# Optimization experiments

Hardware: AMD Instinct MI355X
Metric: run time of the kernel (lower is better)

The kernel has to match this reference:

```python
import jax, jax.numpy as jnp
import numpy as np

PAD = 1  # PAD_token; embedding rows at PAD are zero (padding_idx)


def setup_inputs() -> dict:
    V, D, HOPS = 50000, 128, 3
    B, Lc, Mc = 16, 256, 8
    Lk, Mk = 512, 8
    key = jax.random.key(0)
    kC, kK, kc, kk = jax.random.split(key, 4)
    # one table per hop (C_0..C_{HOPS-1}, K_0..K_{HOPS-1}), init N(0, 0.1)
    C = 0.1 * jax.random.normal(kC, (HOPS, V, D), dtype=jnp.float32)
    K = 0.1 * jax.random.normal(kK, (HOPS, V, D), dtype=jnp.float32)
    C = C.at[:, PAD].set(0.0)
    K = K.at[:, PAD].set(0.0)
    conv_seqs = jax.random.randint(kc, (B, Lc, Mc), 0, V)
    kb_arr = jax.random.randint(kk, (B, Lk, Mk), 0, V)  # dense, PAD-padded ragged KB
    return {"conv_seqs": conv_seqs, "kb_arr": kb_arr, "C": C, "K": K}


def reference(conv_seqs, kb_arr, C, K):
    B, Lc, _ = conv_seqs.shape
    HOPS, _, D = C.shape
    conv_feature = jnp.zeros((B, Lc, D), dtype=C.dtype)
    for hop in range(HOPS):
        # embedding-bag: gather + sum over span tokens
        cf = jnp.sum(C[hop][conv_seqs], axis=2)  # [B, Lc, D]
        kf = jnp.sum(K[hop][kb_arr], axis=2)     # [B, Lk, D]
        att = jnp.einsum('bld,bkd->blk', cf, kf)  # [B, Lc, Lk]
        p = jax.nn.softmax(att, axis=-1)
        conv_feature = jnp.einsum('blk,bkd->bld', p, kf) + conv_feature
    return conv_feature.transpose(1, 0, 2)  # [Lc, B, D]
```

## Files before the change

kernel.cpp:

```cpp
#include <hip/hip_runtime.h>

#define V_    50000
#define D_    128
#define HOPS_ 3
#define B_    16
#define LC_   256
#define MC_   8
#define LK_   512
#define MK_   8

typedef __bf16  bf16x8  __attribute__((ext_vector_type(8)));
typedef unsigned short ushort8 __attribute__((ext_vector_type(8)));
typedef unsigned short ushort4v __attribute__((ext_vector_type(4)));
typedef float   floatx4 __attribute__((ext_vector_type(4)));

__device__ inline unsigned short f2bf(float f) {
    union { float f; unsigned u; } x; x.f = f;
    unsigned r = x.u + 0x7FFFu + ((x.u >> 16) & 1u);
    return (unsigned short)(r >> 16);
}

__device__ inline floatx4 mfma_bf16(ushort8 a, ushort8 b, floatx4 c) {
    return __builtin_amdgcn_mfma_f32_16x16x32_bf16(
        __builtin_bit_cast(bf16x8, a), __builtin_bit_cast(bf16x8, b), c, 0, 0, 0);
}

__global__ __launch_bounds__(256, 6) void gather_kernel(
    const int* __restrict__ kb_arr, const float* __restrict__ Kt,
    unsigned short* __restrict__ kf, unsigned short* __restrict__ kfT,
    float4* __restrict__ out4)
{
    __shared__ unsigned short tile[16][136];

    const int tid  = threadIdx.x;
    const int bx   = blockIdx.x;

    constexpr int KBLK = HOPS_ * B_ * (LK_ / 16);

    if (bx >= KBLK) {
        out4[(size_t)(bx - KBLK) * 256 + tid] = make_float4(0.f, 0.f, 0.f, 0.f);
        return;
    }

    const int r    = tid >> 4;
    const int s    = tid & 15;
    const int lane = tid & 63;

    const int hop  = bx / (B_ * 32);
    const int rem  = bx % (B_ * 32);
    const int b    = rem >> 5;
    const int row0 = (rem & 31) * 16;
    const int g    = hop * B_ + b;

    const int* idxp = kb_arr + (size_t)(b * LK_ + row0 + r) * MK_;
    const float* table = Kt + (size_t)hop * V_ * D_;
    unsigned short* dst = kf + ((size_t)g * LK_ + row0 + r) * D_;

    const int myidx = idxp[s & 7];
    int idxs[8];
    #pragma unroll
    for (int m = 0; m < 8; ++m)
        idxs[m] = __shfl(myidx, (lane & 48) + m);

    float4 a0 = make_float4(0.f, 0.f, 0.f, 0.f);
    float4 a1 = make_float4(0.f, 0.f, 0.f, 0.f);

    #pragma unroll
    for (int m = 0; m < 8; ++m) {
        const float4* rowp = (const float4*)(table + (size_t)idxs[m] * D_);
        float4 v0 = rowp[s * 2];
        float4 v1 = rowp[s * 2 + 1];
        a0.x += v0.x; a0.y += v0.y; a0.z += v0.z; a0.w += v0.w;
        a1.x += v1.x; a1.y += v1.y; a1.z += v1.z; a1.w += v1.w;
    }

    ushort8 o;
    o[0] = f2bf(a0.x); o[1] = f2bf(a0.y); o[2] = f2bf(a0.z); o[3] = f2bf(a0.w);
    o[4] = f2bf(a1.x); o[5] = f2bf(a1.y); o[6] = f2bf(a1.z); o[7] = f2bf(a1.w);
    *(ushort8*)(dst + s * 8) = o;

    *(ushort8*)&tile[r][s * 8] = o;
    __syncthreads();
    const int d    = tid >> 1;
    const int half = tid & 1;
    unsigned short* tdst = kfT + ((size_t)g * D_ + d) * LK_ + row0 + half * 8;
    ushort8 t8;
    #pragma unroll
    for (int i = 0; i < 8; ++i) t8[i] = tile[half * 8 + i][d];
    *(ushort8*)(tdst) = t8;
}

__global__ __launch_bounds__(512) void attn_kernel(
    const int* __restrict__ conv_seqs, const float* __restrict__ Ct,
    const unsigned short* __restrict__ kf, const unsigned short* __restrict__ kfT,
    float* __restrict__ out)
{
    constexpr int AS = 516;
    constexpr int PS = 520;
    __shared__ float att_s[16][AS];
    __shared__ unsigned short p_s[16][PS];
    __shared__ float rowinv_s[16];

    unsigned short* cf_s = &p_s[0][0];

    const int tid  = threadIdx.x;
    const int wave = tid >> 6;
    const int lane = tid & 63;
    const int quad = lane >> 4;
    const int l16  = lane & 15;

    const int gl  = blockIdx.x & 7;
    const int s_  = blockIdx.x >> 3;
    const int lt  = s_ / 6;
    const int gh  = s_ % 6;
    const int g   = gh * 8 + gl;
    const int hop = g >> 4;
    const int b   = g & 15;
    const int l0  = lt * 16;

    const unsigned short* kf_h  = kf  + ((size_t)g) * 512 * 128;
    const unsigned short* kfT_h = kfT + ((size_t)g) * 128 * 512;

    {
        const int bag = tid >> 5;
        const int sl  = tid & 31;
        const int d0  = sl * 4;
        const int* idxp = conv_seqs + (size_t)(b * LC_ + l0 + bag) * MC_;
        const float* table = Ct + (size_t)hop * V_ * D_;
        float4 acc = make_float4(0.f, 0.f, 0.f, 0.f);
        #pragma unroll
        for (int m = 0; m < 8; ++m) {
            const float4 v = *(const float4*)(table + (size_t)idxp[m] * D_ + d0);
            acc.x += v.x; acc.y += v.y; acc.z += v.z; acc.w += v.w;
        }
        ushort4v oc;
        oc[0] = f2bf(acc.x); oc[1] = f2bf(acc.y);
        oc[2] = f2bf(acc.z); oc[3] = f2bf(acc.w);
        *(ushort4v*)&cf_s[bag * 132 + d0] = oc;
    }
    __syncthreads();

    ushort8 afrag[4];
    #pragma unroll
    for (int ks = 0; ks < 4; ++ks)
        afrag[ks] = *(const ushort8*)&cf_s[l16 * 132 + ks * 32 + quad * 8];

    #pragma unroll
    for (int t = 0; t < 4; ++t) {
        const int nt = wave * 4 + t;
        floatx4 acc = {0.f, 0.f, 0.f, 0.f};
        #pragma unroll
        for (int ks = 0; ks < 4; ++ks) {
            ushort8 bfrag = *(const ushort8*)(kf_h + (nt * 16 + l16) * 128 + ks * 32 + quad * 8);
            acc = mfma_bf16(afrag[ks], bfrag, acc);
        }
        #pragma unroll
        for (int rr = 0; rr < 4; ++rr)
            att_s[quad * 4 + rr][nt * 16 + l16] = acc[rr];
    }
    __syncthreads();

    #pragma unroll
    for (int rr = 0; rr < 2; ++rr) {
        const int row = wave * 2 + rr;
        float v[8];
        float mx = -1e30f;
        #pragma unroll
        for (int j = 0; j < 8; ++j) {
            v[j] = att_s[row][lane + j * 64];
            mx = fmaxf(mx, v[j]);
        }
        #pragma unroll
        for (int off = 32; off; off >>= 1) mx = fmaxf(mx, __shfl_xor(mx, off));
        float sum = 0.f;
        #pragma unroll
        for (int j = 0; j < 8; ++j) {
            float e = __expf(v[j] - mx);
            p_s[row][lane + j * 64] = f2bf(e);
            sum += e;
        }
        #pragma unroll
        for (int off = 32; off; off >>= 1) sum += __shfl_xor(sum, off);
        if (lane == 0) rowinv_s[row] = 1.0f / sum;
    }
    __syncthreads();

    floatx4 pacc = {0.f, 0.f, 0.f, 0.f};
    #pragma unroll
    for (int ks = 0; ks < 16; ++ks) {
        ushort8 pa    = *(const ushort8*)&p_s[l16][ks * 32 + quad * 8];
        ushort8 bfrag = *(const ushort8*)(kfT_h + (size_t)(wave * 16 + l16) * 512 + ks * 32 + quad * 8);
        pacc = mfma_bf16(pa, bfrag, pacc);
    }

    const int d = wave * 16 + l16;
    #pragma unroll
    for (int rr = 0; rr < 4; ++rr)
        atomicAdd(&out[(((size_t)(l0 + quad * 4 + rr)) * 16 + b) * 128 + d],
                  pacc[rr] * rowinv_s[quad * 4 + rr]);
}

extern "C" void kernel_launch(void* const* d_in, const int* in_sizes, int n_in,
                              void* d_out, int out_size, void* d_ws, size_t ws_size,
                              hipStream_t stream) {
    (void)in_sizes; (void)n_in; (void)out_size; (void)ws_size;
    const int*   conv_seqs = (const int*)d_in[0];
    const int*   kb_arr    = (const int*)d_in[1];
    const float* C         = (const float*)d_in[2];
    const float* K         = (const float*)d_in[3];

    unsigned short* kf  = (unsigned short*)d_ws;
    unsigned short* kfT = kf + (size_t)HOPS_ * B_ * LK_ * D_;
    float* out = (float*)d_out;

    hipLaunchKernelGGL(gather_kernel, dim3(2048), dim3(256), 0, stream,
                       kb_arr, K, kf, kfT, (float4*)out);
    hipLaunchKernelGGL(attn_kernel, dim3(768), dim3(512), 0, stream,
                       conv_seqs, C, kf, kfT, out);
}
```

Before: 189.6 us.

## Fuse KB gather and attention into one cooperative kernel with grid sync

Merges the KB embedding-bag gather, the output zeroing and the attention kernel into a single cooperative launch of 768 blocks. Each block gathers 32 KB rows plus its own 16 conversation bags, then a grid-wide barrier separates gather from attention. The aim is to remove the second launch and the gap between kernels, and to overlap the conv gather with the KB gather. The cost is a grid sync, a requirement that all 768 blocks of 512 threads be co-resident, and a fallback to the two-kernel path if the cooperative launch fails.

```diff
diff --git a/kernel.cpp b/kernel.cpp
--- a/kernel.cpp
+++ b/kernel.cpp
@@ -1,4 +1,7 @@
 #include <hip/hip_runtime.h>
+#include <hip/hip_cooperative_groups.h>
+
+namespace cg = cooperative_groups;
 
 #define V_    50000
 #define D_    128
@@ -23,6 +26,169 @@
 __device__ inline floatx4 mfma_bf16(ushort8 a, ushort8 b, floatx4 c) {
     return __builtin_amdgcn_mfma_f32_16x16x32_bf16(
         __builtin_bit_cast(bf16x8, a), __builtin_bit_cast(bf16x8, b), c, 0, 0, 0);
+}
+
+__global__ __launch_bounds__(512, 6) void fused_kernel(
+    const int* __restrict__ conv_seqs, const int* __restrict__ kb_arr,
+    const float* __restrict__ Ct, const float* __restrict__ Kt,
+    unsigned short* __restrict__ kf, unsigned short* __restrict__ kfT,
+    float* __restrict__ out)
+{
+    constexpr int AS = 516;
+    constexpr int PS = 520;
+    __shared__ float att_s[16][AS];
+    __shared__ unsigned short p_s[16][PS];
+    __shared__ float rowinv_s[16];
+
+    unsigned short* cf_s = (unsigned short*)&att_s[0][0];
+    unsigned short (*tile2)[136] = (unsigned short (*)[136])&p_s[0][0];
+
+    const int tid  = threadIdx.x;
+    const int wave = tid >> 6;
+    const int lane = tid & 63;
+    const int quad = lane >> 4;
+    const int l16  = lane & 15;
+
+    const int gl  = blockIdx.x & 7;
+    const int s_  = blockIdx.x >> 3;
+    const int lt  = s_ / 6;
+    const int gh  = s_ % 6;
+    const int g   = gh * 8 + gl;
+    const int hop = g >> 4;
+    const int b   = g & 15;
+    const int l0  = lt * 16;
+    const int row0 = lt * 32;
+
+    {
+        const int zi = blockIdx.x * 512 + tid;
+        if (zi < LC_ * B_ * D_ / 4)
+            reinterpret_cast<float4*>(out)[zi] = make_float4(0.f, 0.f, 0.f, 0.f);
+    }
+
+    {
+        const int r = tid >> 4;
+        const int s = tid & 15;
+        const int* idxp = kb_arr + (size_t)(b * LK_ + row0 + r) * MK_;
+        const float* table = Kt + (size_t)hop * V_ * D_;
+        unsigned short* dst = kf + ((size_t)g * LK_ + row0 + r) * D_;
+
+        const int myidx = idxp[s & 7];
+        int idxs[8];
+        #pragma unroll
+        for (int m = 0; m < 8; ++m)
+            idxs[m] = __shfl(myidx, (lane & 48) + m);
+
+        float4 a0 = make_float4(0.f, 0.f, 0.f, 0.f);
+        float4 a1 = make_float4(0.f, 0.f, 0.f, 0.f);
+        #pragma unroll
+        for (int m = 0; m < 8; ++m) {
+            const float4* rowp = (const float4*)(table + (size_t)idxs[m] * D_);
+            float4 v0 = rowp[s * 2];
+            float4 v1 = rowp[s * 2 + 1];
+            a0.x += v0.x; a0.y += v0.y; a0.z += v0.z; a0.w += v0.w;
+            a1.x += v1.x; a1.y += v1.y; a1.z += v1.z; a1.w += v1.w;
+        }
+
+        ushort8 o;
+        o[0] = f2bf(a0.x); o[1] = f2bf(a0.y); o[2] = f2bf(a0.z); o[3] = f2bf(a0.w);
+        o[4] = f2bf(a1.x); o[5] = f2bf(a1.y); o[6] = f2bf(a1.z); o[7] = f2bf(a1.w);
+        *(ushort8*)(dst + s * 8) = o;
+        *(ushort8*)&tile2[r][s * 8] = o;
+    }
+
+    {
+        const int bag = tid >> 5;
+        const int sl  = tid & 31;
+        const int d0  = sl * 4;
+        const int* idxp = conv_seqs + (size_t)(b * LC_ + l0 + bag) * MC_;
+        const float* table = Ct + (size_t)hop * V_ * D_;
+        float4 acc = make_float4(0.f, 0.f, 0.f, 0.f);
+        #pragma unroll
+        for (int m = 0; m < 8; ++m) {
+            const float4 v = *(const float4*)(table + (size_t)idxp[m] * D_ + d0);
+            acc.x += v.x; acc.y += v.y; acc.z += v.z; acc.w += v.w;
+        }
+        ushort4v oc;
+        oc[0] = f2bf(acc.x); oc[1] = f2bf(acc.y);
+        oc[2] = f2bf(acc.z); oc[3] = f2bf(acc.w);
+        *(ushort4v*)&cf_s[bag * 132 + d0] = oc;
+    }
+
+    __syncthreads();
+
+    {
+        const int d   = tid >> 2;
+        const int sub = tid & 3;
+        ushort8 t8;
+        #pragma unroll
+        for (int i = 0; i < 8; ++i) t8[i] = tile2[sub * 8 + i][d];
+        *(ushort8*)(kfT + ((size_t)g * D_ + d) * LK_ + row0 + sub * 8) = t8;
+    }
+
+    cg::this_grid().sync();
+
+    const unsigned short* kf_h  = kf  + (size_t)g * LK_ * D_;
+    const unsigned short* kfT_h = kfT + (size_t)g * D_ * LK_;
+
+    ushort8 afrag[4];
+    #pragma unroll
+    for (int ks = 0; ks < 4; ++ks)
+        afrag[ks] = *(const ushort8*)&cf_s[l16 * 132 + ks * 32 + quad * 8];
+    __syncthreads();
+
+    #pragma unroll
+    for (int t = 0; t < 4; ++t) {
+        const int nt = wave * 4 + t;
+        floatx4 acc = {0.f, 0.f, 0.f, 0.f};
+        #pragma unroll
+        for (int ks = 0; ks < 4; ++ks) {
+            ushort8 bfrag = *(const ushort8*)(kf_h + (nt * 16 + l16) * 128 + ks * 32 + quad * 8);
+            acc = mfma_bf16(afrag[ks], bfrag, acc);
+        }
+        #pragma unroll
+        for (int rr = 0; rr < 4; ++rr)
+            att_s[quad * 4 + rr][nt * 16 + l16] = acc[rr];
+    }
+    __syncthreads();
+
+    #pragma unroll
+    for (int rr = 0; rr < 2; ++rr) {
+        const int row = wave * 2 + rr;
+        float v[8];
+        float mx = -1e30f;
+        #pragma unroll
+        for (int j = 0; j < 8; ++j) {
+            v[j] = att_s[row][lane + j * 64];
+            mx = fmaxf(mx, v[j]);
+        }
+        #pragma unroll
+        for (int off = 32; off; off >>= 1) mx = fmaxf(mx, __shfl_xor(mx, off));
+        float sum = 0.f;
+        #pragma unroll
+        for (int j = 0; j < 8; ++j) {
+            float e = __expf(v[j] - mx);
+            p_s[row][lane + j * 64] = f2bf(e);
+            sum += e;
+        }
+        #pragma unroll
+        for (int off = 32; off; off >>= 1) sum += __shfl_xor(sum, off);
+        if (lane == 0) rowinv_s[row] = 1.0f / sum;
+    }
+    __syncthreads();
+
+    floatx4 pacc = {0.f, 0.f, 0.f, 0.f};
+    #pragma unroll
+    for (int ks = 0; ks < 16; ++ks) {
+        ushort8 pa    = *(const ushort8*)&p_s[l16][ks * 32 + quad * 8];
+        ushort8 bfrag = *(const ushort8*)(kfT_h + (size_t)(wave * 16 + l16) * 512 + ks * 32 + quad * 8);
+        pacc = mfma_bf16(pa, bfrag, pacc);
+    }
+
+    const int d = wave * 16 + l16;
+    #pragma unroll
+    for (int rr = 0; rr < 4; ++rr)
+        atomicAdd(&out[(((size_t)(l0 + quad * 4 + rr)) * 16 + b) * 128 + d],
+                  pacc[rr] * rowinv_s[quad * 4 + rr]);
 }
 
 __global__ __launch_bounds__(256, 6) void gather_kernel(
@@ -213,8 +379,23 @@
     unsigned short* kfT = kf + (size_t)HOPS_ * B_ * LK_ * D_;
     float* out = (float*)d_out;
 
-    hipLaunchKernelGGL(gather_kernel, dim3(2048), dim3(256), 0, stream,
-                       kb_arr, K, kf, kfT, (float4*)out);
-    hipLaunchKernelGGL(attn_kernel, dim3(768), dim3(512), 0, stream,
-                       conv_seqs, C, kf, kfT, out);
-}
+    void* args[7];
+    args[0] = (void*)&conv_seqs;
+    args[1] = (void*)&kb_arr;
+    args[2] = (void*)&C;
+    args[3] = (void*)&K;
+    args[4] = (void*)&kf;
+    args[5] = (void*)&kfT;
+    args[6] = (void*)&out;
+
+    hipError_t e = hipLaunchCooperativeKernel(
+        reinterpret_cast<const void*>(&fused_kernel),
+        dim3(768), dim3(512), args, 0, stream);
+
+    if (e != hipSuccess) {
+        hipLaunchKernelGGL(gather_kernel, dim3(2048), dim3(256), 0, stream,
+                           kb_arr, K, kf, kfT, (float4*)out);
+        hipLaunchKernelGGL(attn_kernel, dim3(768), dim3(512), 0, stream,
+                           conv_seqs, C, kf, kfT, out);
+    }
+}
```

Result: slower. 291.0 us (+53.5%).
